# Kernel tuning notes

Measured on AMD Instinct MI355X. Metric: run time of the kernel, lower is better.

The kernel has to match this reference:

```python
import jax, jax.numpy as jnp
import numpy as np

VOCAB, EMB, H, NLAB, L = 128000, 300, 250, 5, 32


def setup_inputs() -> dict:
    key = jax.random.key(0)
    ks = jax.random.split(key, 24)
    rn = lambda k, s, sc: jax.random.normal(k, s, jnp.float32) * sc
    return {
        "x1": jax.random.randint(ks[0], (1, L), 0, VOCAB),
        "x2": jax.random.randint(ks[1], (1, L), 0, VOCAB),
        "embedding": rn(ks[2], (VOCAB, EMB), 1.0),
        "w_ih": rn(ks[3], (4 * H, EMB), 0.04),
        "w_hh": rn(ks[4], (4 * H, H), 0.06),
        "b_ih": jnp.zeros((4 * H,), jnp.float32),
        "b_hh": jnp.zeros((4 * H,), jnp.float32),
        "cw1": rn(ks[5], (128, 12, 3, 3), 0.1), "cb1": jnp.zeros((128,)),
        "cw2": rn(ks[6], (164, 128, 3, 3), 0.03), "cb2": jnp.zeros((164,)),
        "cw3": rn(ks[7], (192, 164, 3, 3), 0.026), "cb3": jnp.zeros((192,)),
        "cw4": rn(ks[8], (192, 192, 3, 3), 0.024), "cb4": jnp.zeros((192,)),
        "cw5": rn(ks[9], (128, 192, 3, 3), 0.024), "cb5": jnp.zeros((128,)),
        "dnn_w": rn(ks[10], (128, 128), 0.09), "dnn_b": jnp.zeros((128,)),
        "out_w": rn(ks[11], (NLAB, 128), 0.09), "out_b": jnp.zeros((NLAB,)),
    }


def _lstm(xs, w_ih, w_hh, b_ih, b_hh):
    # PyTorch LSTM, single layer; gate order i,f,g,o. xs: [L, EMB] -> [L, H]
    h_dim = w_hh.shape[1]

    def step(carry, x):
        h, c = carry
        g = x @ w_ih.T + h @ w_hh.T + b_ih + b_hh
        i, f, gg, o = jnp.split(g, 4)
        c = jax.nn.sigmoid(f) * c + jax.nn.sigmoid(i) * jnp.tanh(gg)
        h = jax.nn.sigmoid(o) * jnp.tanh(c)
        return (h, c), h

    z = jnp.zeros((h_dim,), xs.dtype)
    _, hs = jax.lax.scan(step, (z, z), xs)
    return hs


def _sim3(a, b):
    # a: [n1, D], b: [n2, D] -> [3, n1, n2] (dot, cosine, l2 distance)
    dot = a @ b.T
    cos = dot / (jnp.linalg.norm(a, axis=1)[:, None] * jnp.linalg.norm(b, axis=1)[None, :] + 1e-8)
    l2 = jnp.linalg.norm(a[:, None, :] - b[None, :, :], axis=2)
    return jnp.stack([dot, cos, l2], 0)


def _greedy_mask(sim2d):
    # Greedy one-to-one bipartite matching over the top (n1+n2) entries.
    n1, n2 = sim2d.shape
    k = min(n1 + n2, n1 * n2)
    _, idx = jax.lax.top_k(sim2d.reshape(-1), k)

    def step(carry, ind):
        s1, s2, sel = carry
        p1, p2 = ind // n2, ind % n2
        ok = jnp.logical_not(s1[p1] | s2[p2])
        s1 = s1.at[p1].set(s1[p1] | ok)
        s2 = s2.at[p2].set(s2[p2] | ok)
        sel = sel.at[p1, p2].set(sel[p1, p2] | ok)
        return (s1, s2, sel), None

    init = (jnp.zeros((n1,), bool), jnp.zeros((n2,), bool), jnp.zeros((n1, n2), bool))
    (_, _, sel), _ = jax.lax.scan(step, init, idx)
    return sel


def reference(x1, x2, embedding, w_ih, w_hh, b_ih, b_hh, cw1, cb1, cw2, cb2, cw3, cb3,
              cw4, cb4, cw5, cb5, dnn_w, dnn_b, out_w, out_b):
    lstm = lambda e: _lstm(e, w_ih, w_hh, b_ih, b_hh)
    bienc = lambda e: jnp.concatenate([lstm(e), lstm(e[::-1])], axis=1)  # [L, 2H]
    s1, s2 = bienc(embedding[x1[0]]), bienc(embedding[x2[0]])
    sim_cube = jnp.concatenate([
        _sim3(s1, s2),
        _sim3(s1[:, :H], s2[:, :H]),
        _sim3(s1[:, H:], s2[:, H:]),
        _sim3(s1[:, :H] + s1[:, H:], s2[:, :H] + s2[:, H:]),
    ], 0)[:, :32, :32]  # [12, 32, 32]
    sel = _greedy_mask(sim_cube[9]) | _greedy_mask(sim_cube[10])
    focus = jnp.where(sel, 1.0, 0.1)[None] * sim_cube
    x = focus[None]  # [1, 12, 32, 32]

    conv = lambda x, w, b: jax.lax.conv_general_dilated(
        x, w, (1, 1), 'SAME', dimension_numbers=('NCHW', 'OIHW', 'NCHW')) + b[None, :, None, None]
    pool = lambda x: jax.lax.reduce_window(x, -jnp.inf, jax.lax.max, (1, 1, 2, 2), (1, 1, 2, 2), 'VALID')
    x = pool(jax.nn.relu(conv(x, cw1, cb1)))   # 32 -> 16
    x = pool(jax.nn.relu(conv(x, cw2, cb2)))   # 16 -> 8
    x = pool(jax.nn.relu(conv(x, cw3, cb3)))   # 8 -> 4
    x = pool(jax.nn.relu(conv(x, cw4, cb4)))   # 4 -> 2
    x = pool(jax.nn.relu(conv(x, cw5, cb5)))   # 2 -> 1
    x = jax.nn.relu(x.reshape(1, -1) @ dnn_w.T + dnn_b)
    return x @ out_w.T + out_b
```

## Files before the change

kernel.cpp:

```cpp
#include <hip/hip_runtime.h>
#include <hip/hip_bf16.h>
#include <hip/hip_fp16.h>

#define DI __device__ __forceinline__
typedef unsigned int uint;
typedef __attribute__((ext_vector_type(2))) _Float16 v2h;
typedef __attribute__((ext_vector_type(2))) __fp16 v2hf;

DI float bf2f(unsigned short b) { return __uint_as_float(((unsigned)b) << 16); }
DI float bf2f_lo(uint u) { return __uint_as_float(u << 16); }
DI float bf2f_hi(uint u) { return __uint_as_float(u & 0xffff0000u); }
DI float sigm(float x) { return 1.0f / (1.0f + expf(-x)); }

DI float ldf(const void* p, int i, int f32) {
  return f32 ? ((const float*)p)[i] : bf2f(((const unsigned short*)p)[i]);
}

DI float dot2(uint w, uint h, float acc) {
#if __has_builtin(__builtin_amdgcn_fdot2)
  return __builtin_amdgcn_fdot2(__builtin_bit_cast(v2h, w),
                                __builtin_bit_cast(v2h, h), acc, false);
#else
  __half2 a = __builtin_bit_cast(__half2, w), b = __builtin_bit_cast(__half2, h);
  acc = fmaf(__half2float(a.x), __half2float(b.x), acc);
  return fmaf(__half2float(a.y), __half2float(b.y), acc);
#endif
}

DI uint pack2(float a, float b) {
#if __has_builtin(__builtin_amdgcn_cvt_pkrtz)
  v2hf p = __builtin_amdgcn_cvt_pkrtz(a, b);
  return __builtin_bit_cast(uint, p);
#else
  __half2 p = __floats2half2_rn(a, b);
  return __builtin_bit_cast(uint, p);
#endif
}

constexpr int OFF_P    = 0;
constexpr int OFF_S    = 64000;
constexpr int OFF_SIM  = 96000;
constexpr int OFF_A0   = 108288;
constexpr int OFF_A1   = 120576;
constexpr int OFF_A2   = 153344;
constexpr int OFF_A3   = 163840;
constexpr int OFF_A4   = 166912;
constexpr int OFF_A5   = 167680;
constexpr int OFF_WT1  = 167936;
constexpr int OFF_WT2  = 181760;
constexpr int OFF_WT3  = 370688;
constexpr int OFF_WT4  = 654080;
constexpr int OFF_WT5  = 985856;
constexpr int OFF_WHH  = 1207040;
constexpr int OFF_FLAG = 1335040;
constexpr int OFF_CB   = 1335048;
constexpr int OFF_DNNW = 1336328;
constexpr int OFF_DNNB = 1352712;
constexpr int OFF_OUTW = 1352840;
constexpr int OFF_OUTB = 1353480;

__global__ __launch_bounds__(256) void k_mode(const uint4* __restrict__ w4,
                                              int* __restrict__ flag) {
  __shared__ int cnt;
  if (threadIdx.x == 0) cnt = 0;
  __syncthreads();
  int c = 0;
  for (int i = threadIdx.x; i < 8192; i += 256) {
    uint4 v = w4[i];
    uint a[4] = {v.x, v.y, v.z, v.w};
#pragma unroll
    for (int q = 0; q < 4; ++q) {
      if ((a[q] & 0x00007F80u) == 0x00007F80u) c++;
      if ((a[q] & 0x7F800000u) == 0x7F800000u) c++;
    }
  }
  atomicAdd(&cnt, c);
  __syncthreads();
  if (threadIdx.x == 0) *flag = (cnt > 0) ? 1 : 0;
}

template <int CI>
DI void wt_tr(int gid, int stride, int N, float* dst, const void* src, int f32) {
  for (int i = gid; i < N; i += stride) {
    int oc  = i / (9 * CI);
    int r   = i - oc * 9 * CI;
    int ci  = r / 9;
    int tap = r - ci * 9;
    dst[(oc * 9 + tap) * CI + ci] = ldf(src, i, f32);
  }
}

DI void cvt_arr(int gid, int stride, int n, float* dst, const void* src, int f32) {
  for (int i = gid; i < n; i += stride) dst[i] = ldf(src, i, f32);
}

__global__ __launch_bounds__(256) void k_prep(
    const int* __restrict__ x1, const int* __restrict__ x2,
    const void* __restrict__ emb, const void* __restrict__ wih, const void* __restrict__ whh,
    const void* __restrict__ bih, const void* __restrict__ bhh,
    const void* __restrict__ cw1, const void* __restrict__ cw2, const void* __restrict__ cw3,
    const void* __restrict__ cw4, const void* __restrict__ cw5,
    const void* __restrict__ cb1, const void* __restrict__ cb2, const void* __restrict__ cb3,
    const void* __restrict__ cb4, const void* __restrict__ cb5,
    const void* __restrict__ dnnw, const void* __restrict__ dnnb,
    const void* __restrict__ outw, const void* __restrict__ outb,
    float* __restrict__ ws, __half* __restrict__ whh_h, const int* __restrict__ flagp) {
  int f32 = *flagp;
  __shared__ __align__(16) float e[300];
  int b = blockIdx.x, tid = threadIdx.x;
  if (b < 64) {
    int s = b >> 5, t = b & 31;
    int tok = (s == 0 ? x1 : x2)[t];
    for (int i = tid; i < 300; i += 256) e[i] = ldf(emb, tok * 300 + i, f32);
    __syncthreads();
    float* P = ws + OFF_P + (s * 32 + t) * 1000;
    if (f32) {
      const float* W = (const float*)wih;
      for (int row = tid; row < 1000; row += 256) {
        float acc = ((const float*)bih)[row] + ((const float*)bhh)[row];
        const float* wr = W + row * 300;
#pragma unroll 4
        for (int k = 0; k < 300; ++k) acc = fmaf(wr[k], e[k], acc);
        P[row] = acc;
      }
    } else {
      const float2* e2 = (const float2*)e;
      for (int row = tid; row < 1000; row += 256) {
        float acc = ldf(bih, row, 0) + ldf(bhh, row, 0);
        const uint* wr = (const uint*)((const unsigned short*)wih + row * 300);
#pragma unroll 10
        for (int m = 0; m < 150; ++m) {
          uint u = wr[m];
          float2 ev = e2[m];
          acc = fmaf(bf2f_lo(u), ev.x, acc);
          acc = fmaf(bf2f_hi(u), ev.y, acc);
        }
        P[row] = acc;
      }
    }
  } else {
    int gid = (b - 64) * 256 + tid;
    const int stride = 64 * 256;
    for (int i = gid; i < 250000; i += stride) {
      int row = i / 250, col = i - row * 250;
      whh_h[row * 256 + col] = __float2half(ldf(whh, i, f32));
    }
    wt_tr<12>(gid, stride, 13824, ws + OFF_WT1, cw1, f32);
    wt_tr<128>(gid, stride, 188928, ws + OFF_WT2, cw2, f32);
    wt_tr<164>(gid, stride, 283392, ws + OFF_WT3, cw3, f32);
    wt_tr<192>(gid, stride, 331776, ws + OFF_WT4, cw4, f32);
    wt_tr<192>(gid, stride, 221184, ws + OFF_WT5, cw5, f32);
    cvt_arr(gid, stride, 128, ws + OFF_CB + 0 * 256, cb1, f32);
    cvt_arr(gid, stride, 164, ws + OFF_CB + 1 * 256, cb2, f32);
    cvt_arr(gid, stride, 192, ws + OFF_CB + 2 * 256, cb3, f32);
    cvt_arr(gid, stride, 192, ws + OFF_CB + 3 * 256, cb4, f32);
    cvt_arr(gid, stride, 128, ws + OFF_CB + 4 * 256, cb5, f32);
    cvt_arr(gid, stride, 16384, ws + OFF_DNNW, dnnw, f32);
    cvt_arr(gid, stride, 128, ws + OFF_DNNB, dnnb, f32);
    cvt_arr(gid, stride, 640, ws + OFF_OUTW, outw, f32);
    cvt_arr(gid, stride, 5, ws + OFF_OUTB, outb, f32);
  }
}

__global__ __launch_bounds__(1024) void k_lstm(
    const float* __restrict__ P_all, const __half* __restrict__ Wp,
    float* __restrict__ S) {
  __shared__ __align__(16) uint2 wl[7][1000];
  __shared__ __align__(16) uint h2[128];
  __shared__ __align__(16) float gates[1000];
  int tid = threadIdx.x;
  int r = blockIdx.x, s = r >> 1, rev = r & 1;
  bool act = tid < 1000;
  const uint* wrow = (const uint*)(Wp + tid * 256);

  uint4 wq[24];
  if (act) {
    const uint4* w4 = (const uint4*)wrow;
#pragma unroll
    for (int j = 0; j < 24; ++j) wq[j] = w4[j];
    const uint2* w2 = (const uint2*)wrow;
#pragma unroll
    for (int j = 0; j < 7; ++j) wl[j][tid] = w2[48 + j];
  }
  if (tid < 128) h2[tid] = 0u;
  float c = 0.0f;
  __syncthreads();

  const float* P = P_all + s * 32000;
#pragma unroll 1
  for (int t = 0; t < 32; ++t) {
    int tp = rev ? (31 - t) : t;
    if (act) {
      float acc = P[tp * 1000 + tid];
      uint2 ta = *(const uint2*)(wrow + 110);
      uint4 tb = *(const uint4*)(wrow + 112);
      uint4 tc = *(const uint4*)(wrow + 116);
      uint4 td = *(const uint4*)(wrow + 120);
      uint  te = wrow[124];
      const uint4* h4 = (const uint4*)h2;
#pragma unroll
      for (int j = 0; j < 24; ++j) {
        uint4 hv = h4[j];
        acc = dot2(wq[j].x, hv.x, acc);
        acc = dot2(wq[j].y, hv.y, acc);
        acc = dot2(wq[j].z, hv.z, acc);
        acc = dot2(wq[j].w, hv.w, acc);
      }
#pragma unroll
      for (int j = 0; j < 7; ++j) {
        uint2 wv = wl[j][tid];
        acc = dot2(wv.x, h2[96 + 2 * j], acc);
        acc = dot2(wv.y, h2[97 + 2 * j], acc);
      }
      acc = dot2(ta.x, h2[110], acc);
      acc = dot2(ta.y, h2[111], acc);
      acc = dot2(tb.x, h2[112], acc);
      acc = dot2(tb.y, h2[113], acc);
      acc = dot2(tb.z, h2[114], acc);
      acc = dot2(tb.w, h2[115], acc);
      acc = dot2(tc.x, h2[116], acc);
      acc = dot2(tc.y, h2[117], acc);
      acc = dot2(tc.z, h2[118], acc);
      acc = dot2(tc.w, h2[119], acc);
      acc = dot2(td.x, h2[120], acc);
      acc = dot2(td.y, h2[121], acc);
      acc = dot2(td.z, h2[122], acc);
      acc = dot2(td.w, h2[123], acc);
      acc = dot2(te,   h2[124], acc);
      gates[tid] = acc;
    }
    __syncthreads();
    if (tid < 250) {
      float gi = gates[tid], gf = gates[250 + tid];
      float gg = gates[500 + tid], go = gates[750 + tid];
      c = sigm(gf) * c + sigm(gi) * tanhf(gg);
      float hn = sigm(go) * tanhf(c);
      S[(s * 32 + t) * 500 + rev * 250 + tid] = hn;
      float ho = __shfl_down(hn, 1);
      if ((tid & 1) == 0) h2[tid >> 1] = pack2(hn, ho);
    }
    __syncthreads();
  }
}

__global__ __launch_bounds__(64) void k_sim(const float* __restrict__ S,
                                            float* __restrict__ SIM) {
  int i = blockIdx.x >> 5, j = blockIdx.x & 31, l = threadIdx.x;
  const float* a = S + i * 500;
  const float* bv = S + 16000 + j * 500;
  float d[10];
#pragma unroll
  for (int v = 0; v < 10; ++v) d[v] = 0.0f;
  for (int k = l; k < 250; k += 64) {
    float af = a[k], ab = a[250 + k], bf = bv[k], bb = bv[250 + k];
    d[0] = fmaf(af, bf, d[0]);  d[1] = fmaf(ab, bb, d[1]);
    d[2] = fmaf(af, bb, d[2]);  d[3] = fmaf(ab, bf, d[3]);
    d[4] = fmaf(af, af, d[4]);  d[5] = fmaf(ab, ab, d[5]);
    d[6] = fmaf(af, ab, d[6]);  d[7] = fmaf(bf, bf, d[7]);
    d[8] = fmaf(bb, bb, d[8]);  d[9] = fmaf(bf, bb, d[9]);
  }
#pragma unroll
  for (int v = 0; v < 10; ++v)
    for (int off = 32; off > 0; off >>= 1) d[v] += __shfl_down(d[v], off);
  if (l == 0) {
    float dff = d[0], dbb = d[1], dfb = d[2], dbf = d[3];
    float nf1 = d[4], nb1 = d[5], c1 = d[6], nf2 = d[7], nb2 = d[8], c2 = d[9];
    int p = i * 32 + j;
    float dot = dff + dbb, n1f = nf1 + nb1, n2f = nf2 + nb2;
    SIM[0 * 1024 + p] = dot;
    SIM[1 * 1024 + p] = dot / (sqrtf(n1f) * sqrtf(n2f) + 1e-8f);
    SIM[2 * 1024 + p] = sqrtf(fmaxf(n1f + n2f - 2.0f * dot, 0.0f));
    SIM[3 * 1024 + p] = dff;
    SIM[4 * 1024 + p] = dff / (sqrtf(nf1) * sqrtf(nf2) + 1e-8f);
    SIM[5 * 1024 + p] = sqrtf(fmaxf(nf1 + nf2 - 2.0f * dff, 0.0f));
    SIM[6 * 1024 + p] = dbb;
    SIM[7 * 1024 + p] = dbb / (sqrtf(nb1) * sqrtf(nb2) + 1e-8f);
    SIM[8 * 1024 + p] = sqrtf(fmaxf(nb1 + nb2 - 2.0f * dbb, 0.0f));
    float dsum = dff + dbb + dfb + dbf;
    float ns1 = n1f + 2.0f * c1, ns2 = n2f + 2.0f * c2;
    SIM[9 * 1024 + p] = dsum;
    SIM[10 * 1024 + p] = dsum / (sqrtf(ns1) * sqrtf(ns2) + 1e-8f);
    SIM[11 * 1024 + p] = sqrtf(fmaxf(ns1 + ns2 - 2.0f * dsum, 0.0f));
  }
}

__global__ __launch_bounds__(1024) void k_greedy(const float* __restrict__ SIM,
                                                 float* __restrict__ A0) {
  __shared__ unsigned long long keys[1024];
  __shared__ unsigned char sel[1024];
  int t = threadIdx.x;
  sel[t] = 0;
  for (int ch = 0; ch < 2; ++ch) {
    float v = SIM[(9 + ch) * 1024 + t];
    uint u = __float_as_uint(v);
    u = (u & 0x80000000u) ? ~u : (u | 0x80000000u);
    keys[t] = (((unsigned long long)u) << 32) | (uint)(1023 - t);
    __syncthreads();
    for (int k = 2; k <= 1024; k <<= 1) {
      for (int j = k >> 1; j > 0; j >>= 1) {
        int ixj = t ^ j;
        if (ixj > t) {
          unsigned long long a = keys[t], b2 = keys[ixj];
          bool desc = ((t & k) == 0);
          if ((a < b2) == desc) { keys[t] = b2; keys[ixj] = a; }
        }
        __syncthreads();
      }
    }
    if (t == 0) {
      uint m1 = 0, m2 = 0;
      for (int n = 0; n < 64; ++n) {
        int flat = 1023 - (int)(keys[n] & 0xFFFFFFFFu);
        int p1 = flat >> 5, p2 = flat & 31;
        if (!((m1 >> p1) & 1u) && !((m2 >> p2) & 1u)) {
          m1 |= 1u << p1; m2 |= 1u << p2; sel[flat] = 1;
        }
      }
    }
    __syncthreads();
  }
  float fac = sel[t] ? 1.0f : 0.1f;
#pragma unroll
  for (int cidx = 0; cidx < 12; ++cidx)
    A0[t * 12 + cidx] = SIM[cidx * 1024 + t] * fac;
}

template <int CIN, int CP, int COUT, int WIN, int TILESX, int G>
__global__ __launch_bounds__(256) void k_conv_tiled(
    const float* __restrict__ in, const float* __restrict__ wt,
    const float* __restrict__ bias, float* __restrict__ out) {
  __shared__ __align__(16) float lin[100 * CP];
  __shared__ float pbuf[G * 64];
  int tid = threadIdx.x, b = blockIdx.x;
  const int TILES = TILESX * TILESX;
  int tile = b % TILES, ocg = b / TILES;
  int ty = tile / TILESX, tx = tile % TILESX;
  int oc0 = ocg * G;
  const int NQ = 25 * CIN;
  for (int m = tid; m < NQ; m += 256) {
    int pxy = m / (CIN / 4), cq = m - pxy * (CIN / 4);
    int py = pxy / 10, px = pxy - py * 10;
    int gy = ty * 8 + py - 1, gx = tx * 8 + px - 1;
    float4 v = make_float4(0.f, 0.f, 0.f, 0.f);
    if (gy >= 0 && gy < WIN && gx >= 0 && gx < WIN)
      v = *(const float4*)(in + (gy * WIN + gx) * CIN + 4 * cq);
    *(float4*)(lin + (py * 10 + px) * CP + 4 * cq) = v;
  }
  __syncthreads();
  int px = tid & 63, ocl = tid >> 6;
  int py2 = px >> 3, px2 = px & 7;
  const int G4 = G / 4;
  float acc[G4];
  int ocw[G4];
#pragma unroll
  for (int m = 0; m < G4; ++m) {
    int oc = oc0 + ocl + 4 * m;
    ocw[m] = (oc < COUT) ? oc : (COUT - 1);
    acc[m] = (oc < COUT) ? bias[oc] : 0.0f;
  }
#pragma unroll
  for (int tap = 0; tap < 9; ++tap) {
    int ky = tap / 3, kx = tap % 3;
    const float* ibase = lin + ((py2 + ky) * 10 + (px2 + kx)) * CP;
#pragma unroll 4
    for (int cq = 0; cq < CIN / 4; ++cq) {
      float4 iv = *(const float4*)(ibase + 4 * cq);
#pragma unroll
      for (int m = 0; m < G4; ++m) {
        float4 wv = *(const float4*)(wt + (ocw[m] * 9 + tap) * CIN + 4 * cq);
        acc[m] = fmaf(iv.x, wv.x, fmaf(iv.y, wv.y, fmaf(iv.z, wv.z, fmaf(iv.w, wv.w, acc[m]))));
      }
    }
  }
#pragma unroll
  for (int m = 0; m < G4; ++m)
    pbuf[(ocl + 4 * m) * 64 + px] = fmaxf(acc[m], 0.0f);
  __syncthreads();
  if (tid < G * 16) {
    int ocl2 = tid >> 4, q = tid & 15;
    int qy = q >> 2, qx = q & 3;
    const float* pb = pbuf + ocl2 * 64 + qy * 16 + qx * 2;
    float v = fmaxf(fmaxf(pb[0], pb[1]), fmaxf(pb[8], pb[9]));
    int oc = oc0 + ocl2;
    if (oc < COUT) {
      int gy = ty * 4 + qy, gx = tx * 4 + qx;
      out[(gy * (WIN / 2) + gx) * COUT + oc] = v;
    }
  }
}

template <int CIN, int CP, int COUT, int HW, int G>
__global__ __launch_bounds__(256) void k_conv_small(
    const float* __restrict__ in, const float* __restrict__ wt,
    const float* __restrict__ bias, float* __restrict__ out) {
  __shared__ __align__(16) float lin[HW * HW * CP];
  __shared__ float pbuf[G * HW * HW];
  int tid = threadIdx.x;
  int oc0 = blockIdx.x * G;
  const int NPX = HW * HW;
  const int NQ = NPX * CIN / 4;
  for (int m = tid; m < NQ; m += 256) {
    int pxy = m / (CIN / 4), cq = m - pxy * (CIN / 4);
    float4 v = *(const float4*)(in + pxy * CIN + 4 * cq);
    *(float4*)(lin + pxy * CP + 4 * cq) = v;
  }
  __syncthreads();
  int px = tid % NPX, ocl = tid / NPX;
  int py = px / HW, pxx = px % HW;
  int oc = oc0 + ocl;
  float acc = bias[oc];
#pragma unroll
  for (int tap = 0; tap < 9; ++tap) {
    int yy = py + tap / 3 - 1, xx = pxx + tap % 3 - 1;
    if (yy >= 0 && yy < HW && xx >= 0 && xx < HW) {
      const float* ibase = lin + (yy * HW + xx) * CP;
      const float* wbase = wt + (oc * 9 + tap) * CIN;
#pragma unroll 4
      for (int cq = 0; cq < CIN / 4; ++cq) {
        float4 iv = *(const float4*)(ibase + 4 * cq);
        float4 wv = *(const float4*)(wbase + 4 * cq);
        acc = fmaf(iv.x, wv.x, fmaf(iv.y, wv.y, fmaf(iv.z, wv.z, fmaf(iv.w, wv.w, acc))));
      }
    }
  }
  pbuf[ocl * NPX + px] = fmaxf(acc, 0.0f);
  __syncthreads();
  const int HW2 = HW / 2;
  if (tid < G * HW2 * HW2) {
    int ocl2 = tid / (HW2 * HW2), q = tid % (HW2 * HW2);
    int qy = q / HW2, qx = q % HW2;
    const float* pb = pbuf + ocl2 * NPX + (2 * qy) * HW + 2 * qx;
    float v = fmaxf(fmaxf(pb[0], pb[1]), fmaxf(pb[HW], pb[HW + 1]));
    out[(qy * HW2 + qx) * COUT + oc0 + ocl2] = v;
  }
}

__global__ __launch_bounds__(256) void k_fc(
    const float* __restrict__ A5,
    const float* __restrict__ dnnw, const float* __restrict__ dnnb,
    const float* __restrict__ outw, const float* __restrict__ outb,
    const int* __restrict__ flagp, void* __restrict__ outp) {
  __shared__ __align__(16) float v[128], u[128];
  int t = threadIdx.x;
  if (t < 128) v[t] = A5[t];
  __syncthreads();
  if (t < 128) {
    float acc = dnnb[t];
    const float* wr = dnnw + t * 128;
#pragma unroll 8
    for (int k = 0; k < 128; ++k) acc = fmaf(wr[k], v[k], acc);
    u[t] = fmaxf(acc, 0.0f);
  }
  __syncthreads();
  if (t < 5) {
    float acc = outb[t];
    const float* wr = outw + t * 128;
#pragma unroll 8
    for (int k = 0; k < 128; ++k) acc = fmaf(wr[k], u[k], acc);
    if (*flagp) ((float*)outp)[t] = acc;
    else ((__hip_bfloat16*)outp)[t] = __float2bfloat16(acc);
  }
}

extern "C" void kernel_launch(void* const* d_in, const int* in_sizes, int n_in,
                              void* d_out, int out_size, void* d_ws, size_t ws_size,
                              hipStream_t stream) {
  const int* x1 = (const int*)d_in[0];
  const int* x2 = (const int*)d_in[1];

  float* ws = (float*)d_ws;
  __half* whh_h = (__half*)(ws + OFF_WHH);
  int* flagp = (int*)(ws + OFF_FLAG);

  k_mode<<<1, 256, 0, stream>>>((const uint4*)d_in[4], flagp);
  k_prep<<<128, 256, 0, stream>>>(x1, x2,
      d_in[2], d_in[3], d_in[4], d_in[5], d_in[6],
      d_in[7], d_in[9], d_in[11], d_in[13], d_in[15],
      d_in[8], d_in[10], d_in[12], d_in[14], d_in[16],
      d_in[17], d_in[18], d_in[19], d_in[20],
      ws, whh_h, flagp);
  k_lstm<<<4, 1024, 0, stream>>>(ws + OFF_P, whh_h, ws + OFF_S);
  k_sim<<<1024, 64, 0, stream>>>(ws + OFF_S, ws + OFF_SIM);
  k_greedy<<<1, 1024, 0, stream>>>(ws + OFF_SIM, ws + OFF_A0);
  k_conv_tiled<12, 12, 128, 32, 4, 8><<<256, 256, 0, stream>>>(ws + OFF_A0, ws + OFF_WT1, ws + OFF_CB + 0 * 256, ws + OFF_A1);
  k_conv_tiled<128, 132, 164, 16, 2, 8><<<84, 256, 0, stream>>>(ws + OFF_A1, ws + OFF_WT2, ws + OFF_CB + 1 * 256, ws + OFF_A2);
  k_conv_small<164, 164, 192, 8, 4><<<48, 256, 0, stream>>>(ws + OFF_A2, ws + OFF_WT3, ws + OFF_CB + 2 * 256, ws + OFF_A3);
  k_conv_small<192, 196, 192, 4, 16><<<12, 256, 0, stream>>>(ws + OFF_A3, ws + OFF_WT4, ws + OFF_CB + 3 * 256, ws + OFF_A4);
  k_conv_small<192, 196, 128, 2, 64><<<2, 256, 0, stream>>>(ws + OFF_A4, ws + OFF_WT5, ws + OFF_CB + 4 * 256, ws + OFF_A5);
  k_fc<<<1, 256, 0, stream>>>(ws + OFF_A5, ws + OFF_DNNW, ws + OFF_DNNB,
                              ws + OFF_OUTW, ws + OFF_OUTB, flagp, d_out);
}
```

Before: 645.9 us.

## Split prep into tiled input-projection GEMM and per-channel weight transpose kernels

The monolithic prep kernel is split in two. One is a dedicated input-projection kernel with 125 blocks that stages embedding rows and W_ih rows in shared memory, so every token reuses each weight row. The other transposes the conv weights one output channel per block through shared memory, giving coalesced reads and writes, and runs across 868 blocks. The greedy kernel now sorts both similarity channels in one bitonic pass and runs both greedy scans at once, and the mode-check kernel uses 1024 threads. This adds a kernel launch but spreads the previously serialized, uncoalesced prep work over many more blocks.

```diff
diff --git a/kernel.cpp b/kernel.cpp
--- a/kernel.cpp
+++ b/kernel.cpp
@@ -4,6 +4,7 @@
 
 #define DI __device__ __forceinline__
 typedef unsigned int uint;
+typedef unsigned long long ull;
 typedef __attribute__((ext_vector_type(2))) _Float16 v2h;
 typedef __attribute__((ext_vector_type(2))) __fp16 v2hf;
 
@@ -59,13 +60,13 @@
 constexpr int OFF_OUTW = 1352840;
 constexpr int OFF_OUTB = 1353480;
 
-__global__ __launch_bounds__(256) void k_mode(const uint4* __restrict__ w4,
-                                              int* __restrict__ flag) {
+__global__ __launch_bounds__(1024) void k_mode(const uint4* __restrict__ w4,
+                                               int* __restrict__ flag) {
   __shared__ int cnt;
   if (threadIdx.x == 0) cnt = 0;
   __syncthreads();
   int c = 0;
-  for (int i = threadIdx.x; i < 8192; i += 256) {
+  for (int i = threadIdx.x; i < 8192; i += 1024) {
     uint4 v = w4[i];
     uint a[4] = {v.x, v.y, v.z, v.w};
 #pragma unroll
@@ -79,25 +80,69 @@
   if (threadIdx.x == 0) *flag = (cnt > 0) ? 1 : 0;
 }
 
-template <int CI>
-DI void wt_tr(int gid, int stride, int N, float* dst, const void* src, int f32) {
-  for (int i = gid; i < N; i += stride) {
-    int oc  = i / (9 * CI);
-    int r   = i - oc * 9 * CI;
-    int ci  = r / 9;
-    int tap = r - ci * 9;
-    dst[(oc * 9 + tap) * CI + ci] = ldf(src, i, f32);
-  }
+__global__ __launch_bounds__(256) void k_pgemm(
+    const int* __restrict__ x1, const int* __restrict__ x2,
+    const void* __restrict__ emb, const void* __restrict__ wih,
+    const void* __restrict__ bih, const void* __restrict__ bhh,
+    float* __restrict__ P, const int* __restrict__ flagp) {
+  int f32 = *flagp;
+  __shared__ int toks[64];
+  __shared__ __align__(16) float e_lds[64 * 102];
+  __shared__ __align__(16) float w_lds[8 * 102];
+  int tid = threadIdx.x, n = blockIdx.x;
+  if (tid < 64) toks[tid] = (tid < 32) ? x1[tid] : x2[tid - 32];
+  __syncthreads();
+  int tok = tid & 63, r2 = tid >> 6;
+  int row0 = 8 * n + r2, row1 = row0 + 4;
+  float a0 = 0.f, a1 = 0.f;
+  for (int kc = 0; kc < 300; kc += 100) {
+    for (int idx = tid; idx < 6400; idx += 256) {
+      int tk = idx / 100, kk = idx - tk * 100;
+      e_lds[tk * 102 + kk] = ldf(emb, toks[tk] * 300 + kc + kk, f32);
+    }
+    for (int idx = tid; idx < 800; idx += 256) {
+      int rr = idx >> 7 , kk2 = idx & 127;
+      rr = idx / 100; kk2 = idx - rr * 100;
+      w_lds[rr * 102 + kk2] = ldf(wih, (8 * n + rr) * 300 + kc + kk2, f32);
+    }
+    __syncthreads();
+    const float2* ep  = (const float2*)(e_lds + tok * 102);
+    const float2* w0p = (const float2*)(w_lds + r2 * 102);
+    const float2* w1p = (const float2*)(w_lds + (r2 + 4) * 102);
+#pragma unroll 10
+    for (int m = 0; m < 50; ++m) {
+      float2 ev = ep[m];
+      float2 wa = w0p[m], wb = w1p[m];
+      a0 = fmaf(ev.x, wa.x, a0); a0 = fmaf(ev.y, wa.y, a0);
+      a1 = fmaf(ev.x, wb.x, a1); a1 = fmaf(ev.y, wb.y, a1);
+    }
+    __syncthreads();
+  }
+  a0 += ldf(bih, row0, f32) + ldf(bhh, row0, f32);
+  a1 += ldf(bih, row1, f32) + ldf(bhh, row1, f32);
+  P[tok * 1000 + row0] = a0;
+  P[tok * 1000 + row1] = a1;
 }
 
 DI void cvt_arr(int gid, int stride, int n, float* dst, const void* src, int f32) {
   for (int i = gid; i < n; i += stride) dst[i] = ldf(src, i, f32);
 }
 
-__global__ __launch_bounds__(256) void k_prep(
-    const int* __restrict__ x1, const int* __restrict__ x2,
-    const void* __restrict__ emb, const void* __restrict__ wih, const void* __restrict__ whh,
-    const void* __restrict__ bih, const void* __restrict__ bhh,
+template <int CI>
+DI void oc_tr(int ocl, float* __restrict__ dst, const void* __restrict__ src,
+              int f32, float* lds, int tid) {
+  const int N = CI * 9;
+  int base = ocl * N;
+  for (int m = tid; m < N; m += 256) lds[m] = ldf(src, base + m, f32);
+  __syncthreads();
+  for (int j = tid; j < N; j += 256) {
+    int tap = j / CI, ci = j - tap * CI;
+    dst[base + j] = lds[ci * 9 + tap];
+  }
+}
+
+__global__ __launch_bounds__(256) void k_pwt(
+    const void* __restrict__ whh,
     const void* __restrict__ cw1, const void* __restrict__ cw2, const void* __restrict__ cw3,
     const void* __restrict__ cw4, const void* __restrict__ cw5,
     const void* __restrict__ cb1, const void* __restrict__ cb2, const void* __restrict__ cb3,
@@ -106,50 +151,20 @@
     const void* __restrict__ outw, const void* __restrict__ outb,
     float* __restrict__ ws, __half* __restrict__ whh_h, const int* __restrict__ flagp) {
   int f32 = *flagp;
-  __shared__ __align__(16) float e[300];
+  __shared__ __align__(16) float lds[1728];
   int b = blockIdx.x, tid = threadIdx.x;
-  if (b < 64) {
-    int s = b >> 5, t = b & 31;
-    int tok = (s == 0 ? x1 : x2)[t];
-    for (int i = tid; i < 300; i += 256) e[i] = ldf(emb, tok * 300 + i, f32);
-    __syncthreads();
-    float* P = ws + OFF_P + (s * 32 + t) * 1000;
-    if (f32) {
-      const float* W = (const float*)wih;
-      for (int row = tid; row < 1000; row += 256) {
-        float acc = ((const float*)bih)[row] + ((const float*)bhh)[row];
-        const float* wr = W + row * 300;
-#pragma unroll 4
-        for (int k = 0; k < 300; ++k) acc = fmaf(wr[k], e[k], acc);
-        P[row] = acc;
-      }
-    } else {
-      const float2* e2 = (const float2*)e;
-      for (int row = tid; row < 1000; row += 256) {
-        float acc = ldf(bih, row, 0) + ldf(bhh, row, 0);
-        const uint* wr = (const uint*)((const unsigned short*)wih + row * 300);
-#pragma unroll 10
-        for (int m = 0; m < 150; ++m) {
-          uint u = wr[m];
-          float2 ev = e2[m];
-          acc = fmaf(bf2f_lo(u), ev.x, acc);
-          acc = fmaf(bf2f_hi(u), ev.y, acc);
-        }
-        P[row] = acc;
-      }
-    }
-  } else {
-    int gid = (b - 64) * 256 + tid;
+  if (b < 128)      oc_tr<12>(b, ws + OFF_WT1, cw1, f32, lds, tid);
+  else if (b < 292) oc_tr<128>(b - 128, ws + OFF_WT2, cw2, f32, lds, tid);
+  else if (b < 484) oc_tr<164>(b - 292, ws + OFF_WT3, cw3, f32, lds, tid);
+  else if (b < 676) oc_tr<192>(b - 484, ws + OFF_WT4, cw4, f32, lds, tid);
+  else if (b < 804) oc_tr<192>(b - 676, ws + OFF_WT5, cw5, f32, lds, tid);
+  else {
+    int gid = (b - 804) * 256 + tid;
     const int stride = 64 * 256;
     for (int i = gid; i < 250000; i += stride) {
       int row = i / 250, col = i - row * 250;
       whh_h[row * 256 + col] = __float2half(ldf(whh, i, f32));
     }
-    wt_tr<12>(gid, stride, 13824, ws + OFF_WT1, cw1, f32);
-    wt_tr<128>(gid, stride, 188928, ws + OFF_WT2, cw2, f32);
-    wt_tr<164>(gid, stride, 283392, ws + OFF_WT3, cw3, f32);
-    wt_tr<192>(gid, stride, 331776, ws + OFF_WT4, cw4, f32);
-    wt_tr<192>(gid, stride, 221184, ws + OFF_WT5, cw5, f32);
     cvt_arr(gid, stride, 128, ws + OFF_CB + 0 * 256, cb1, f32);
     cvt_arr(gid, stride, 164, ws + OFF_CB + 1 * 256, cb2, f32);
     cvt_arr(gid, stride, 192, ws + OFF_CB + 2 * 256, cb3, f32);
@@ -286,39 +301,45 @@
 
 __global__ __launch_bounds__(1024) void k_greedy(const float* __restrict__ SIM,
                                                  float* __restrict__ A0) {
-  __shared__ unsigned long long keys[1024];
+  __shared__ ull keys0[1024], keys1[1024];
   __shared__ unsigned char sel[1024];
   int t = threadIdx.x;
   sel[t] = 0;
-  for (int ch = 0; ch < 2; ++ch) {
-    float v = SIM[(9 + ch) * 1024 + t];
-    uint u = __float_as_uint(v);
-    u = (u & 0x80000000u) ? ~u : (u | 0x80000000u);
-    keys[t] = (((unsigned long long)u) << 32) | (uint)(1023 - t);
-    __syncthreads();
-    for (int k = 2; k <= 1024; k <<= 1) {
-      for (int j = k >> 1; j > 0; j >>= 1) {
-        int ixj = t ^ j;
-        if (ixj > t) {
-          unsigned long long a = keys[t], b2 = keys[ixj];
-          bool desc = ((t & k) == 0);
-          if ((a < b2) == desc) { keys[t] = b2; keys[ixj] = a; }
-        }
-        __syncthreads();
+  {
+    float v0 = SIM[9 * 1024 + t], v1 = SIM[10 * 1024 + t];
+    uint u0 = __float_as_uint(v0);
+    u0 = (u0 & 0x80000000u) ? ~u0 : (u0 | 0x80000000u);
+    uint u1 = __float_as_uint(v1);
+    u1 = (u1 & 0x80000000u) ? ~u1 : (u1 | 0x80000000u);
+    keys0[t] = (((ull)u0) << 32) | (uint)(1023 - t);
+    keys1[t] = (((ull)u1) << 32) | (uint)(1023 - t);
+  }
+  __syncthreads();
+  for (int k = 2; k <= 1024; k <<= 1) {
+    for (int j = k >> 1; j > 0; j >>= 1) {
+      int ixj = t ^ j;
+      if (ixj > t) {
+        bool desc = ((t & k) == 0);
+        ull a = keys0[t], b2 = keys0[ixj];
+        if ((a < b2) == desc) { keys0[t] = b2; keys0[ixj] = a; }
+        ull c2 = keys1[t], d2 = keys1[ixj];
+        if ((c2 < d2) == desc) { keys1[t] = d2; keys1[ixj] = c2; }
       }
-    }
-    if (t == 0) {
-      uint m1 = 0, m2 = 0;
-      for (int n = 0; n < 64; ++n) {
-        int flat = 1023 - (int)(keys[n] & 0xFFFFFFFFu);
-        int p1 = flat >> 5, p2 = flat & 31;
-        if (!((m1 >> p1) & 1u) && !((m2 >> p2) & 1u)) {
-          m1 |= 1u << p1; m2 |= 1u << p2; sel[flat] = 1;
-        }
+      __syncthreads();
+    }
+  }
+  if (t == 0 || t == 512) {
+    const ull* ks = (t == 0) ? keys0 : keys1;
+    uint m1 = 0, m2 = 0;
+    for (int n = 0; n < 64; ++n) {
+      int flat = 1023 - (int)(ks[n] & 0xFFFFFFFFu);
+      int p1 = flat >> 5, p2 = flat & 31;
+      if (!((m1 >> p1) & 1u) && !((m2 >> p2) & 1u)) {
+        m1 |= 1u << p1; m2 |= 1u << p2; sel[flat] = 1;
       }
     }
-    __syncthreads();
-  }
+  }
+  __syncthreads();
   float fac = sel[t] ? 1.0f : 0.1f;
 #pragma unroll
   for (int cidx = 0; cidx < 12; ++cidx)
@@ -472,9 +493,10 @@
   __half* whh_h = (__half*)(ws + OFF_WHH);
   int* flagp = (int*)(ws + OFF_FLAG);
 
-  k_mode<<<1, 256, 0, stream>>>((const uint4*)d_in[4], flagp);
-  k_prep<<<128, 256, 0, stream>>>(x1, x2,
-      d_in[2], d_in[3], d_in[4], d_in[5], d_in[6],
+  k_mode<<<1, 1024, 0, stream>>>((const uint4*)d_in[4], flagp);
+  k_pgemm<<<125, 256, 0, stream>>>(x1, x2, d_in[2], d_in[3], d_in[5], d_in[6],
+                                   ws + OFF_P, flagp);
+  k_pwt<<<868, 256, 0, stream>>>(d_in[4],
       d_in[7], d_in[9], d_in[11], d_in[13], d_in[15],
       d_in[8], d_in[10], d_in[12], d_in[14], d_in[16],
       d_in[17], d_in[18], d_in[19], d_in[20],
```

Result: faster. 562.3 us (-12.9%).
